# Kernel optimization log

Hardware: AMD Instinct MI355X
Metric: run time of the kernel (lower is better)

## Reference

```python
import jax, jax.numpy as jnp
import numpy as np

B, T, LAT = 32, 196, 256
NJ3, NJ2, NJ1 = 13, 10, 20  # joints with feature dims 3, 2, 1 (contiguous groups)
D3, D2, D1 = NJ3 * 3, NJ2 * 2, NJ1 * 1  # spans in the flat feature axis (39, 20, 20)


def setup_inputs() -> dict:
    key = jax.random.key(0)
    ks = jax.random.split(key, 13)
    s = 0.05
    return {
        "x": jax.random.normal(ks[0], (B, T, D3 + D2 + D1), dtype=jnp.float32),
        "W1_3": jax.random.normal(ks[1], (NJ3, 3, LAT), dtype=jnp.float32) * s,
        "b1_3": jax.random.normal(ks[2], (NJ3, LAT), dtype=jnp.float32) * s,
        "W2_3": jax.random.normal(ks[3], (NJ3, LAT, LAT), dtype=jnp.float32) * s,
        "b2_3": jax.random.normal(ks[4], (NJ3, LAT), dtype=jnp.float32) * s,
        "W1_2": jax.random.normal(ks[5], (NJ2, 2, LAT), dtype=jnp.float32) * s,
        "b1_2": jax.random.normal(ks[6], (NJ2, LAT), dtype=jnp.float32) * s,
        "W2_2": jax.random.normal(ks[7], (NJ2, LAT, LAT), dtype=jnp.float32) * s,
        "b2_2": jax.random.normal(ks[8], (NJ2, LAT), dtype=jnp.float32) * s,
        "W1_1": jax.random.normal(ks[9], (NJ1, 1, LAT), dtype=jnp.float32) * s,
        "b1_1": jax.random.normal(ks[10], (NJ1, LAT), dtype=jnp.float32) * s,
        "W2_1": jax.random.normal(ks[11], (NJ1, LAT, LAT), dtype=jnp.float32) * s,
        "b2_1": jax.random.normal(ks[12], (NJ1, LAT), dtype=jnp.float32) * s,
    }


def _group_mlp(xg, W1, b1, W2, b2):
    # xg: [B,T,J,d] ; W1: [J,d,LAT] ; W2: [J,LAT,LAT]
    h = jnp.einsum("btjd,jdl->btjl", xg, W1) + b1
    h = jax.nn.gelu(h)
    return jnp.einsum("btjl,jlm->btjm", h, W2) + b2


def reference(x, W1_3, b1_3, W2_3, b2_3, W1_2, b1_2, W2_2, b2_2, W1_1, b1_1, W2_1, b2_1):
    Bx, Tx, _ = x.shape
    # split the flat feature axis per joint_feature_dims and reshape into [B,T,J,d] groups
    x3 = x[..., :D3].reshape(Bx, Tx, NJ3, 3)
    x2 = x[..., D3:D3 + D2].reshape(Bx, Tx, NJ2, 2)
    x1 = x[..., D3 + D2:].reshape(Bx, Tx, NJ1, 1)
    o3 = _group_mlp(x3, W1_3, b1_3, W2_3, b2_3)
    o2 = _group_mlp(x2, W1_2, b1_2, W2_2, b2_2)
    o1 = _group_mlp(x1, W1_1, b1_1, W2_1, b2_1)
    # stack per-joint outputs in joint order -> [B,T,43,LAT]
    return jnp.concatenate([o3, o2, o1], axis=2)
```

## Files before the change

### kernel.cpp

```cpp
#include <hip/hip_runtime.h>
#include <stdint.h>

#define BT   6272
#define LAT  256
#define NJ3  13
#define NJ2  10
#define NJ1  20
#define NJ   43
#define D3   39
#define D2   20
#define XDIM 79
#define OUTROW 11008
#define NWG  (NJ * 98)

typedef _Float16 half8  __attribute__((ext_vector_type(8)));
typedef _Float16 half4v __attribute__((ext_vector_type(4)));
typedef float    floatx4 __attribute__((ext_vector_type(4)));

__device__ __forceinline__ float fast_gelu(float h) {
    float p  = h * h;
    float u2 = h * (2.3022164464f + 0.1029435704f * p);
    float e  = __builtin_amdgcn_exp2f(u2);
    float r  = __builtin_amdgcn_rcpf(e + 1.0f);
    return h - h * r;
}

__global__ __launch_bounds__(256) void transpose_w2(
    const float* __restrict__ W2_3, const float* __restrict__ W2_2,
    const float* __restrict__ W2_1, _Float16* __restrict__ W2t)
{
    __shared__ float tile[64][65];
    const int bid = blockIdx.x;
    const int j   = bid >> 4;
    const int t   = bid & 15;
    const int l0  = (t >> 2) * 64;
    const int m0  = (t & 3) * 64;

    const float* W2 = (j < NJ3) ? (W2_3 + (size_t)j * 65536)
                    : (j < NJ3 + NJ2) ? (W2_2 + (size_t)(j - NJ3) * 65536)
                    : (W2_1 + (size_t)(j - NJ3 - NJ2) * 65536);

    const int tx = threadIdx.x & 15, ty = threadIdx.x >> 4;
#pragma unroll
    for (int rr = 0; rr < 4; ++rr) {
        const int row = ty + rr * 16;
        const float4 v = *(const float4*)(W2 + (size_t)(l0 + row) * 256 + m0 + tx * 4);
        tile[row][tx * 4 + 0] = v.x;
        tile[row][tx * 4 + 1] = v.y;
        tile[row][tx * 4 + 2] = v.z;
        tile[row][tx * 4 + 3] = v.w;
    }
    __syncthreads();
#pragma unroll
    for (int rr = 0; rr < 4; ++rr) {
        const int mrow = ty + rr * 16;
        const int ll   = tx * 4;
        half4v o;
        o[0] = (_Float16)tile[ll + 0][mrow];
        o[1] = (_Float16)tile[ll + 1][mrow];
        o[2] = (_Float16)tile[ll + 2][mrow];
        o[3] = (_Float16)tile[ll + 3][mrow];
        *(half4v*)(W2t + ((size_t)j * 256 + m0 + mrow) * 256 + l0 + ll) = o;
    }
}

__global__ __launch_bounds__(512, 4) void motion_main(
    const float* __restrict__ x,
    const float* __restrict__ W1_3, const float* __restrict__ b1_3, const float* __restrict__ b2_3,
    const float* __restrict__ W1_2, const float* __restrict__ b1_2, const float* __restrict__ b2_2,
    const float* __restrict__ W1_1, const float* __restrict__ b1_1, const float* __restrict__ b2_1,
    const _Float16* __restrict__ W2t,
    float* __restrict__ out)
{
    __shared__ half8 Alds[2][512];
    __shared__ float W1s[3 * 256];
    __shared__ float b1s[256];

    const int orig = blockIdx.x;
    const int q8   = NWG >> 3, r8 = NWG & 7;
    const int xcd  = orig & 7;
    const int wgid = (xcd < r8 ? xcd * (q8 + 1)
                               : r8 * (q8 + 1) + (xcd - r8) * q8) + (orig >> 3);

    const int j   = wgid / 98;
    const int mt  = wgid % 98;
    const int r0  = mt * 64;

    int d, xoff;
    const float *W1, *b1, *b2;
    if (j < NJ3)            { d = 3; xoff = j * 3;
                              W1 = W1_3 + j * 768;  b1 = b1_3 + j * 256;  b2 = b2_3 + j * 256; }
    else if (j < NJ3 + NJ2) { const int qj = j - NJ3; d = 2; xoff = D3 + qj * 2;
                              W1 = W1_2 + qj * 512;  b1 = b1_2 + qj * 256;  b2 = b2_2 + qj * 256; }
    else                    { const int qj = j - NJ3 - NJ2; d = 1; xoff = D3 + D2 + qj;
                              W1 = W1_1 + qj * 256;  b1 = b1_1 + qj * 256;  b2 = b2_1 + qj * 256; }

    const int tid  = threadIdx.x;
    const int rr   = tid >> 3;
    const int qq   = tid & 7;
    const int lane = tid & 63;
    const int wv   = tid >> 6;
    const int m16  = lane & 15;
    const int quad = lane >> 4;

    const float* W1r0 = W1;
    const float* W1r1 = W1 + ((d > 1) ? 256 : 0);
    const float* W1r2 = W1 + ((d > 2) ? 512 : 0);

    if (tid < 192) {
        const float* src = (tid < 64) ? W1r0 : (tid < 128) ? W1r1 : W1r2;
        const int o = (tid & 63) * 4;
        *(float4*)(W1s + (tid >> 6) * 256 + o) = *(const float4*)(src + o);
    } else if (tid < 256) {
        const int o = (tid - 192) * 4;
        *(float4*)(b1s + o) = *(const float4*)(b1 + o);
    }

    const float* xr  = x + (size_t)(r0 + rr) * XDIM + xoff;
    const float  xv0 = xr[0];
    const float  xv1 = (d > 1) ? xr[1] : 0.0f;
    const float  xv2 = (d > 2) ? xr[2] : 0.0f;

    floatx4 acc[4][2];
#pragma unroll
    for (int i = 0; i < 4; ++i)
#pragma unroll
        for (int jj = 0; jj < 2; ++jj)
            acc[i][jj] = (floatx4){0.f, 0.f, 0.f, 0.f};

    const _Float16* W2j = W2t + (size_t)j * 65536 + (size_t)(wv * 32) * 256;

    auto compute_h = [&](int kc, int nb) {
        const int c  = qq;
        const int l0 = kc * 64 + c * 8;
        float h[8];
#pragma unroll
        for (int u = 0; u < 8; ++u) h[u] = b1s[l0 + u];
#pragma unroll
        for (int u = 0; u < 8; ++u) h[u] += xv0 * W1s[l0 + u];
#pragma unroll
        for (int u = 0; u < 8; ++u) h[u] += xv1 * W1s[256 + l0 + u];
#pragma unroll
        for (int u = 0; u < 8; ++u) h[u] += xv2 * W1s[512 + l0 + u];
        half8 v;
#pragma unroll
        for (int u = 0; u < 8; ++u) v[u] = (_Float16)fast_gelu(h[u]);
        const int slot = (((rr >> 4) * 2 + (c >> 2)) * 4 + (c & 3));
        Alds[nb][slot * 16 + ((rr & 15) ^ ((slot & 3) << 1))] = v;
    };

    __syncthreads();
    compute_h(0, 0);
    __syncthreads();

    for (int kc = 0; kc < 4; ++kc) {
        const int b = kc & 1;
        if (kc < 3) compute_h(kc + 1, b ^ 1);
#pragma unroll
        for (int kk2 = 0; kk2 < 2; ++kk2) {
            half8 af[4];
#pragma unroll
            for (int i = 0; i < 4; ++i) {
                const int slot = (i * 2 + kk2) * 4 + quad;
                af[i] = Alds[b][slot * 16 + (m16 ^ ((slot & 3) << 1))];
            }
            const int kidx = kc * 64 + kk2 * 32 + quad * 8;
            __builtin_amdgcn_s_setprio(1);
#pragma unroll
            for (int jj = 0; jj < 2; ++jj) {
                const half8 bf = *(const half8*)(W2j + (size_t)(jj * 16 + m16) * 256 + kidx);
#pragma unroll
                for (int i = 0; i < 4; ++i)
                    acc[i][jj] = __builtin_amdgcn_mfma_f32_16x16x32_f16(bf, af[i], acc[i][jj], 0, 0, 0);
            }
            __builtin_amdgcn_s_setprio(0);
        }
        if (kc < 3) __syncthreads();
    }

    floatx4 b2q[2];
#pragma unroll
    for (int jj = 0; jj < 2; ++jj)
        b2q[jj] = *(const floatx4*)(b2 + wv * 32 + jj * 16 + quad * 4);

    const size_t colbase = (size_t)j * 256 + wv * 32 + quad * 4;
#pragma unroll
    for (int i = 0; i < 4; ++i) {
        float* orow = out + (size_t)(r0 + i * 16 + m16) * OUTROW + colbase;
#pragma unroll
        for (int jj = 0; jj < 2; ++jj) {
            floatx4 v = acc[i][jj] + b2q[jj];
            __builtin_nontemporal_store(v, (floatx4*)(orow + jj * 16));
        }
    }
}

extern "C" void kernel_launch(void* const* d_in, const int* in_sizes, int n_in,
                              void* d_out, int out_size, void* d_ws, size_t ws_size,
                              hipStream_t stream) {
    const float* x    = (const float*)d_in[0];
    const float* W1_3 = (const float*)d_in[1];
    const float* b1_3 = (const float*)d_in[2];
    const float* W2_3 = (const float*)d_in[3];
    const float* b2_3 = (const float*)d_in[4];
    const float* W1_2 = (const float*)d_in[5];
    const float* b1_2 = (const float*)d_in[6];
    const float* W2_2 = (const float*)d_in[7];
    const float* b2_2 = (const float*)d_in[8];
    const float* W1_1 = (const float*)d_in[9];
    const float* b1_1 = (const float*)d_in[10];
    const float* W2_1 = (const float*)d_in[11];
    const float* b2_1 = (const float*)d_in[12];
    float* out = (float*)d_out;
    _Float16* W2t = (_Float16*)d_ws;

    transpose_w2<<<NJ * 16, 256, 0, stream>>>(W2_3, W2_2, W2_1, W2t);
    motion_main<<<NWG, 512, 0, stream>>>(x, W1_3, b1_3, b2_3,
                                         W1_2, b1_2, b2_2,
                                         W1_1, b1_1, b2_1, W2t, out);
}
```

Measured before the change: 381.8 us.

## Compute full hidden tile upfront and retile waves into 2x4 output grid

The GELU hidden activations for the whole 64x256 tile are now computed once into a single LDS buffer before the GEMM, replacing the double-buffered per-chunk pipeline and its per-iteration barriers. Waves are regrouped as 2 row-groups by 4 column-quarters (32 rows by 64 columns each) instead of each wave owning 32 columns across all 64 rows. This halves the A-fragment LDS reads per MFMA and removes the syncs inside the loop, but the activation compute no longer overlaps with the MFMA work, and the larger LDS footprint may reduce occupancy.

```diff
diff --git a/kernel.cpp b/kernel.cpp
--- a/kernel.cpp
+++ b/kernel.cpp
@@ -72,7 +72,7 @@
     const _Float16* __restrict__ W2t,
     float* __restrict__ out)
 {
-    __shared__ half8 Alds[2][512];
+    __shared__ half8 A2[2048];
     __shared__ float W1s[3 * 256];
     __shared__ float b1s[256];
 
@@ -96,8 +96,6 @@
                               W1 = W1_1 + qj * 256;  b1 = b1_1 + qj * 256;  b2 = b2_1 + qj * 256; }
 
     const int tid  = threadIdx.x;
-    const int rr   = tid >> 3;
-    const int qq   = tid & 7;
     const int lane = tid & 63;
     const int wv   = tid >> 6;
     const int m16  = lane & 15;
@@ -116,80 +114,79 @@
         *(float4*)(b1s + o) = *(const float4*)(b1 + o);
     }
 
-    const float* xr  = x + (size_t)(r0 + rr) * XDIM + xoff;
+    const int wvu = __builtin_amdgcn_readfirstlane(wv);
+    const float* xr  = x + (size_t)(r0 + lane) * XDIM + xoff;
     const float  xv0 = xr[0];
     const float  xv1 = (d > 1) ? xr[1] : 0.0f;
     const float  xv2 = (d > 2) ? xr[2] : 0.0f;
 
-    floatx4 acc[4][2];
-#pragma unroll
-    for (int i = 0; i < 4; ++i)
-#pragma unroll
-        for (int jj = 0; jj < 2; ++jj)
-            acc[i][jj] = (floatx4){0.f, 0.f, 0.f, 0.f};
-
-    const _Float16* W2j = W2t + (size_t)j * 65536 + (size_t)(wv * 32) * 256;
-
-    auto compute_h = [&](int kc, int nb) {
-        const int c  = qq;
-        const int l0 = kc * 64 + c * 8;
-        float h[8];
-#pragma unroll
-        for (int u = 0; u < 8; ++u) h[u] = b1s[l0 + u];
-#pragma unroll
-        for (int u = 0; u < 8; ++u) h[u] += xv0 * W1s[l0 + u];
-#pragma unroll
-        for (int u = 0; u < 8; ++u) h[u] += xv1 * W1s[256 + l0 + u];
-#pragma unroll
-        for (int u = 0; u < 8; ++u) h[u] += xv2 * W1s[512 + l0 + u];
-        half8 v;
-#pragma unroll
-        for (int u = 0; u < 8; ++u) v[u] = (_Float16)fast_gelu(h[u]);
-        const int slot = (((rr >> 4) * 2 + (c >> 2)) * 4 + (c & 3));
-        Alds[nb][slot * 16 + ((rr & 15) ^ ((slot & 3) << 1))] = v;
-    };
-
     __syncthreads();
-    compute_h(0, 0);
+
+    {
+        const int i = lane >> 4, m = lane & 15;
+#pragma unroll
+        for (int t = 0; t < 4; ++t) {
+            const int l0 = wvu * 32 + t * 8;
+            float h[8];
+#pragma unroll
+            for (int u = 0; u < 8; ++u) h[u] = b1s[l0 + u];
+#pragma unroll
+            for (int u = 0; u < 8; ++u) h[u] += xv0 * W1s[l0 + u];
+#pragma unroll
+            for (int u = 0; u < 8; ++u) h[u] += xv1 * W1s[256 + l0 + u];
+#pragma unroll
+            for (int u = 0; u < 8; ++u) h[u] += xv2 * W1s[512 + l0 + u];
+            half8 v;
+#pragma unroll
+            for (int u = 0; u < 8; ++u) v[u] = (_Float16)fast_gelu(h[u]);
+            const int kq = wvu * 4 + t;
+            A2[(i * 32 + kq) * 16 + m] = v;
+        }
+    }
     __syncthreads();
 
+    const int Mg = wv >> 2;
+    const int Nq = wv & 3;
+    const _Float16* W2j = W2t + (size_t)j * 65536 + (size_t)(Nq * 64) * 256;
+
+    floatx4 acc[2][4];
+#pragma unroll
+    for (int i2 = 0; i2 < 2; ++i2)
+#pragma unroll
+        for (int jj = 0; jj < 4; ++jj)
+            acc[i2][jj] = (floatx4){0.f, 0.f, 0.f, 0.f};
+
     for (int kc = 0; kc < 4; ++kc) {
-        const int b = kc & 1;
-        if (kc < 3) compute_h(kc + 1, b ^ 1);
 #pragma unroll
         for (int kk2 = 0; kk2 < 2; ++kk2) {
-            half8 af[4];
-#pragma unroll
-            for (int i = 0; i < 4; ++i) {
-                const int slot = (i * 2 + kk2) * 4 + quad;
-                af[i] = Alds[b][slot * 16 + (m16 ^ ((slot & 3) << 1))];
-            }
+            half8 af[2];
+#pragma unroll
+            for (int i2 = 0; i2 < 2; ++i2)
+                af[i2] = A2[((Mg * 2 + i2) * 32 + kc * 8 + kk2 * 4 + quad) * 16 + m16];
             const int kidx = kc * 64 + kk2 * 32 + quad * 8;
             __builtin_amdgcn_s_setprio(1);
 #pragma unroll
-            for (int jj = 0; jj < 2; ++jj) {
+            for (int jj = 0; jj < 4; ++jj) {
                 const half8 bf = *(const half8*)(W2j + (size_t)(jj * 16 + m16) * 256 + kidx);
-#pragma unroll
-                for (int i = 0; i < 4; ++i)
-                    acc[i][jj] = __builtin_amdgcn_mfma_f32_16x16x32_f16(bf, af[i], acc[i][jj], 0, 0, 0);
+                acc[0][jj] = __builtin_amdgcn_mfma_f32_16x16x32_f16(bf, af[0], acc[0][jj], 0, 0, 0);
+                acc[1][jj] = __builtin_amdgcn_mfma_f32_16x16x32_f16(bf, af[1], acc[1][jj], 0, 0, 0);
             }
             __builtin_amdgcn_s_setprio(0);
         }
-        if (kc < 3) __syncthreads();
-    }
-
-    floatx4 b2q[2];
-#pragma unroll
-    for (int jj = 0; jj < 2; ++jj)
-        b2q[jj] = *(const floatx4*)(b2 + wv * 32 + jj * 16 + quad * 4);
-
-    const size_t colbase = (size_t)j * 256 + wv * 32 + quad * 4;
-#pragma unroll
-    for (int i = 0; i < 4; ++i) {
-        float* orow = out + (size_t)(r0 + i * 16 + m16) * OUTROW + colbase;
-#pragma unroll
-        for (int jj = 0; jj < 2; ++jj) {
-            floatx4 v = acc[i][jj] + b2q[jj];
+    }
+
+    floatx4 b2q[4];
+#pragma unroll
+    for (int jj = 0; jj < 4; ++jj)
+        b2q[jj] = *(const floatx4*)(b2 + Nq * 64 + jj * 16 + quad * 4);
+
+    const size_t colbase = (size_t)j * 256 + Nq * 64 + quad * 4;
+#pragma unroll
+    for (int i2 = 0; i2 < 2; ++i2) {
+        float* orow = out + (size_t)(r0 + Mg * 32 + i2 * 16 + m16) * OUTROW + colbase;
+#pragma unroll
+        for (int jj = 0; jj < 4; ++jj) {
+            floatx4 v = acc[i2][jj] + b2q[jj];
             __builtin_nontemporal_store(v, (floatx4*)(orow + jj * 16));
         }
     }
```

Result: slower. 444.4 us (+16.4%).
